# Performance work log

Measured on AMD Instinct MI355X. Metric: run time of the kernel, lower is better.

## Reference

```python
import jax, jax.numpy as jnp
import numpy as np

L, B, S, D, H = 4, 4, 2048, 512, 8
DH = D // H
FF = 4 * D
BN_EPS = 1e-3  # keras BatchNormalization default epsilon


def setup_inputs() -> dict:
    key = jax.random.key(0)
    ks = jax.random.split(key, 8)
    g = lambda k, shape: jax.random.normal(k, shape, dtype=jnp.float32) * 0.02
    return {
        "sequence": jax.random.normal(ks[0], (B, S, D), dtype=jnp.float32),
        "wq": g(ks[1], (L, D, D)), "bq": jnp.zeros((L, D), jnp.float32),
        "wk": g(ks[2], (L, D, D)), "bk": jnp.zeros((L, D), jnp.float32),
        "wv": g(ks[3], (L, D, D)), "bv": jnp.zeros((L, D), jnp.float32),
        "wo": g(ks[4], (L, D, D)), "bo": jnp.zeros((L, D), jnp.float32),
        "w1": g(ks[5], (L, D, FF)), "b1": jnp.zeros((L, FF), jnp.float32),
        "w2": g(ks[6], (L, FF, D)), "b2": jnp.zeros((L, D), jnp.float32),
        "g1": jnp.ones((L, D), jnp.float32), "be1": jnp.zeros((L, D), jnp.float32),
        "g2": jnp.ones((L, D), jnp.float32), "be2": jnp.zeros((L, D), jnp.float32),
    }


def reference(sequence, wq, bq, wk, bk, wv, bv, wo, bo, w1, b1, w2, b2, g1, be1, g2, be2):
    # Inference-mode BatchNorm with moving_mean=0, moving_var=1:
    # bn(x) = x / sqrt(1 + eps) * gamma + beta
    bn_inv = 1.0 / jnp.sqrt(jnp.float32(1.0 + BN_EPS))
    scale = 1.0 / jnp.sqrt(jnp.float32(DH))
    x = sequence  # [B, S, D]
    for i in range(L):
        # Batched multi-head self-attention (== the per-position loop concat)
        q = (x @ wq[i] + bq[i]).reshape(B, S, H, DH)
        k = (x @ wk[i] + bk[i]).reshape(B, S, H, DH)
        v = (x @ wv[i] + bv[i]).reshape(B, S, H, DH)
        att = jax.nn.softmax(jnp.einsum('bqhd,bkhd->bhqk', q, k) * scale, axis=-1)
        o = jnp.einsum('bhqk,bkhd->bqhd', att, v).reshape(B, S, D)
        o = o @ wo[i] + bo[i]
        x = (x + o) * bn_inv * g1[i] + be1[i]          # residual + BN
        f = jax.nn.relu(x @ w1[i] + b1[i]) @ w2[i] + b2[i]  # FFN
        x = (x + f) * bn_inv * g2[i] + be2[i]          # residual + BN
    return x
```

## Files before the change

kernel.cpp:

```cpp
#include <hip/hip_runtime.h>
#include <hip/hip_bf16.h>

#define BB   4
#define SS   2048
#define DDIM 512
#define HH   8
#define DHD  64
#define FFD  2048
#define LLN  4
#define NQKV 1536
#define BN_INV 0.9995003747f
#define QSCALE 0.18033688011112042f

typedef __bf16 bf16x8 __attribute__((ext_vector_type(8)));
typedef __bf16 bf16x4 __attribute__((ext_vector_type(4)));
typedef float  f32x4  __attribute__((ext_vector_type(4)));
typedef float  f32x16 __attribute__((ext_vector_type(16)));

__device__ __forceinline__ void gl2lds16(const void* g, void* l) {
  __builtin_amdgcn_global_load_lds((const __attribute__((address_space(1))) void*)g,
                                   (__attribute__((address_space(3))) void*)l, 16, 0, 0);
}

__device__ __forceinline__ unsigned pkbf16(float a, float b) {
  union { __bf16 h[2]; unsigned u; } x;
  x.h[0] = (__bf16)a; x.h[1] = (__bf16)b;
  return x.u;
}

__global__ __launch_bounds__(256) void k_transpose_w(const float* __restrict__ in,
                                                     __bf16* __restrict__ out,
                                                     int R, int C,
                                                     size_t in_zs, size_t out_zs) {
  __shared__ float tile[32][33];
  in += (size_t)blockIdx.z * in_zs;
  out += (size_t)blockIdx.z * out_zs;
  const int c0 = blockIdx.x * 32, r0 = blockIdx.y * 32;
  const int tx = threadIdx.x & 31, ty = threadIdx.x >> 5;
#pragma unroll
  for (int k = 0; k < 4; ++k) {
    int r = ty + k * 8;
    tile[r][tx] = in[(size_t)(r0 + r) * C + (c0 + tx)];
  }
  __syncthreads();
#pragma unroll
  for (int k = 0; k < 4; ++k) {
    int c = ty + k * 8;
    out[(size_t)(c0 + c) * R + (r0 + tx)] = (__bf16)tile[tx][c];
  }
}

__global__ __launch_bounds__(256) void k_bias_fuse(const float* __restrict__ bq,
                                                   const float* __restrict__ bk,
                                                   const float* __restrict__ bv,
                                                   float* __restrict__ out) {
  const int i = blockIdx.x * 256 + threadIdx.x;
  const int l = i / NQKV, j = i - l * NQKV;
  float v = (j < 512) ? bq[l * 512 + j]
          : (j < 1024) ? bk[l * 512 + j - 512]
                       : bv[l * 512 + j - 1024];
  out[i] = v;
}

__global__ __launch_bounds__(256) void k_transpose_v(const __bf16* __restrict__ qkv,
                                                     __bf16* __restrict__ vt) {
  __shared__ __bf16 tile[32][33];
  const int s0 = blockIdx.x * 32;
  const int d0 = blockIdx.y * 32;
  const int bh = blockIdx.z, b = bh >> 3, h = bh & 7;
  const int tx = threadIdx.x & 31, ty = threadIdx.x >> 5;
#pragma unroll
  for (int k = 0; k < 4; ++k) {
    int s = ty + k * 8;
    tile[s][tx] = qkv[(size_t)(b * SS + s0 + s) * NQKV + 2 * DDIM + h * DHD + d0 + tx];
  }
  __syncthreads();
#pragma unroll
  for (int k = 0; k < 4; ++k) {
    int d = ty + k * 8;
    vt[(size_t)(bh * DHD + d0 + d) * SS + (s0 + tx)] = tile[tx][d];
  }
}

__global__ __launch_bounds__(256) void k_cast(const float* __restrict__ in,
                                              float* __restrict__ xf,
                                              __bf16* __restrict__ xb) {
  const int i = (blockIdx.x * 256 + threadIdx.x) * 4;
  const float4 v = *(const float4*)(in + i);
  *(float4*)(xf + i) = v;
  bf16x4 o;
  o[0] = (__bf16)v.x; o[1] = (__bf16)v.y; o[2] = (__bf16)v.z; o[3] = (__bf16)v.w;
  *(bf16x4*)(xb + i) = o;
}

template <int EPI>
__global__ __launch_bounds__(256) void k_gemm_bt(const __bf16* __restrict__ A,
                                                 const __bf16* __restrict__ Bt,
                                                 const float* __restrict__ bias,
                                                 __bf16* __restrict__ Cb,
                                                 int M, int N, int K,
                                                 const float* __restrict__ xres,
                                                 float* __restrict__ xout,
                                                 const float* __restrict__ gvec,
                                                 const float* __restrict__ bvec) {
  __shared__ char As[2][16384];
  __shared__ char Bs[2][16384];
  const int tid = threadIdx.x;
  const int l = tid & 63, w = tid >> 6;
  const int wm = w >> 1, wn = w & 1;
  const int m0 = blockIdx.y * 128, n0 = blockIdx.x * 128;
  const int lr = l & 15, lg = l >> 4;
  f32x4 acc[4][4] = {};
  const int nk = K >> 6;
  const size_t ldab = (size_t)K * 2;

  auto stage = [&](int buf, int kt) {
    const int k0b = kt * 128;
#pragma unroll
    for (int i = 0; i < 4; ++i) {
      const int chunk = i * 256 + tid;
      const int row = chunk >> 3;
      const int scb = ((chunk & 7) * 16) ^ ((row & 7) << 4);
      gl2lds16((const char*)A + (size_t)(m0 + row) * ldab + k0b + scb,
               As[buf] + (i * 256 + w * 64) * 16);
      gl2lds16((const char*)Bt + (size_t)(n0 + row) * ldab + k0b + scb,
               Bs[buf] + (i * 256 + w * 64) * 16);
    }
  };

  stage(0, 0);
  __syncthreads();
  int cur = 0;
  for (int kt = 0; kt < nk; ++kt) {
    if (kt + 1 < nk) stage(cur ^ 1, kt + 1);
#pragma unroll
    for (int kk = 0; kk < 2; ++kk) {
      bf16x8 a[4], b[4];
#pragma unroll
      for (int m = 0; m < 4; ++m) {
        const int row = wm * 64 + m * 16 + lr;
        const int cb = kk * 64 + lg * 16;
        a[m] = *(const bf16x8*)(As[cur] + row * 128 + (cb ^ ((row & 7) << 4)));
      }
#pragma unroll
      for (int n = 0; n < 4; ++n) {
        const int row = wn * 64 + n * 16 + lr;
        const int cb = kk * 64 + lg * 16;
        b[n] = *(const bf16x8*)(Bs[cur] + row * 128 + (cb ^ ((row & 7) << 4)));
      }
#pragma unroll
      for (int m = 0; m < 4; ++m)
#pragma unroll
        for (int n = 0; n < 4; ++n)
          acc[m][n] = __builtin_amdgcn_mfma_f32_16x16x32_bf16(a[m], b[n], acc[m][n], 0, 0, 0);
    }
    asm volatile("s_waitcnt vmcnt(0)" ::: "memory");
    __syncthreads();
    cur ^= 1;
  }
#pragma unroll
  for (int m = 0; m < 4; ++m) {
    const int gm = m0 + wm * 64 + m * 16 + lg * 4;
#pragma unroll
    for (int n = 0; n < 4; ++n) {
      const int gn = n0 + wn * 64 + n * 16 + lr;
      const float bv_ = bias[gn];
#pragma unroll
      for (int j = 0; j < 4; ++j) {
        const size_t idx = (size_t)(gm + j) * N + gn;
        float v = acc[m][n][j] + bv_;
        if constexpr (EPI == 1) {
          Cb[idx] = (__bf16)fmaxf(v, 0.0f);
        } else if constexpr (EPI == 2) {
          float t = (xres[idx] + v) * BN_INV * gvec[gn] + bvec[gn];
          xout[idx] = t;
          Cb[idx] = (__bf16)t;
        } else {
          if (gn < DDIM) v *= QSCALE;
          Cb[idx] = (__bf16)v;
        }
      }
    }
  }
}

__global__ __launch_bounds__(256, 2) void k_attn(const __bf16* __restrict__ QKV,
                                                 const __bf16* __restrict__ Vt,
                                                 __bf16* __restrict__ O) {
  __shared__ char smem[65536];
  const int tid = threadIdx.x, l = tid & 63, w = tid >> 6;
  const int lq = l & 31, hi = l >> 5;
  const int f = blockIdx.y * 16 + blockIdx.x;
  const int L = (f & 7) * 64 + (f >> 3);
  const int qt = L & 15, bh = L >> 4;
  const int b = bh >> 3, h = bh & 7;
  const int myq = qt * 128 + w * 32 + lq;
  bf16x8 qf[4];
  {
    const __bf16* qp = QKV + (size_t)(b * SS + myq) * NQKV + h * DHD + hi * 8;
#pragma unroll
    for (int kc = 0; kc < 4; ++kc)
      qf[kc] = *(const bf16x8*)(qp + kc * 16);
  }
  f32x16 oaccT[2] = {};
  float rsum = 0.f;

  auto stage = [&](int buf, int t) {
    const int kv0 = t * 128;
    char* Kd = smem + buf * 16384;
    char* Vd = smem + 32768 + buf * 16384;
#pragma unroll
    for (int i = 0; i < 4; ++i) {
      const int chunk = i * 256 + tid;
      const int row = chunk >> 3;
      const int rs = row ^ ((((row >> 2) + 1) & 2) * 6);
      const int scb = ((chunk & 7) * 16) ^ ((row & 7) << 4);
      gl2lds16((const char*)QKV + ((size_t)(b * SS + kv0 + rs) * NQKV + DDIM + h * DHD) * 2 + scb,
               Kd + (i * 256 + w * 64) * 16);
    }
#pragma unroll
    for (int i = 0; i < 4; ++i) {
      const int chunk = i * 256 + tid;
      const int row = chunk >> 4;
      const int scb = ((chunk & 15) * 16) ^ ((row & 15) << 4);
      gl2lds16((const char*)Vt + ((size_t)(bh * DHD + row) * SS + kv0) * 2 + scb,
               Vd + (i * 256 + w * 64) * 16);
    }
  };

  stage(0, 0);
  __syncthreads();
  int cur = 0;
  for (int t = 0; t < SS / 128; ++t) {
    if (t < SS / 128 - 1) stage(cur ^ 1, t + 1);
    const char* Ks = smem + cur * 16384;
    const char* Vs = smem + 32768 + cur * 16384;
#pragma unroll
    for (int kt2 = 0; kt2 < 4; ++kt2) {
      const int krow = kt2 * 32 + lq;
      const int kswz = (krow & 7) << 4;
      f32x16 st = {};
      __builtin_amdgcn_s_setprio(1);
#pragma unroll
      for (int kc = 0; kc < 4; ++kc) {
        bf16x8 kf = *(const bf16x8*)(Ks + krow * 128 + ((kc * 32 + hi * 16) ^ kswz));
        st = __builtin_amdgcn_mfma_f32_32x32x16_bf16(kf, qf[kc], st, 0, 0, 0);
      }
      __builtin_amdgcn_s_setprio(0);
      unsigned pk8[8];
#pragma unroll
      for (int i = 0; i < 8; ++i) {
        const float e0 = __builtin_amdgcn_exp2f(st[2 * i]);
        const float e1 = __builtin_amdgcn_exp2f(st[2 * i + 1]);
        rsum += e0 + e1;
        pk8[i] = pkbf16(e0, e1);
      }
      union { unsigned u[4]; bf16x8 v; } pf0, pf1;
#pragma unroll
      for (int i = 0; i < 4; ++i) { pf0.u[i] = pk8[i]; pf1.u[i] = pk8[4 + i]; }
      __builtin_amdgcn_s_setprio(1);
#pragma unroll
      for (int dt = 0; dt < 2; ++dt) {
        const int vrow = dt * 32 + lq;
        const int vswz = (vrow & 15) << 4;
        bf16x8 vf0 = *(const bf16x8*)(Vs + vrow * 256 + ((kt2 * 64 + hi * 16) ^ vswz));
        bf16x8 vf1 = *(const bf16x8*)(Vs + vrow * 256 + ((kt2 * 64 + 32 + hi * 16) ^ vswz));
        oaccT[dt] = __builtin_amdgcn_mfma_f32_32x32x16_bf16(vf0, pf0.v, oaccT[dt], 0, 0, 0);
        oaccT[dt] = __builtin_amdgcn_mfma_f32_32x32x16_bf16(vf1, pf1.v, oaccT[dt], 0, 0, 0);
      }
      __builtin_amdgcn_s_setprio(0);
    }
    asm volatile("s_waitcnt vmcnt(0)" ::: "memory");
    __syncthreads();
    cur ^= 1;
  }
  rsum += __shfl_xor(rsum, 32);
  const float inv = 1.0f / rsum;
  __bf16* op = O + (size_t)(b * SS + myq) * DDIM + h * DHD;
#pragma unroll
  for (int dt = 0; dt < 2; ++dt)
#pragma unroll
    for (int g = 0; g < 4; ++g) {
      const int d0 = dt * 32 + g * 8 + hi * 4;
      unsigned u0 = pkbf16(oaccT[dt][4 * g + 0] * inv, oaccT[dt][4 * g + 1] * inv);
      unsigned u1 = pkbf16(oaccT[dt][4 * g + 2] * inv, oaccT[dt][4 * g + 3] * inv);
      uint2 uu; uu.x = u0; uu.y = u1;
      *(uint2*)(op + d0) = uu;
    }
}

static constexpr size_t SZ_WQKVT = (size_t)LLN * NQKV * DDIM * 2;
static constexpr size_t SZ_WOT   = (size_t)LLN * DDIM * DDIM * 2;
static constexpr size_t SZ_WT_DF = (size_t)LLN * DDIM * FFD * 2;
static constexpr size_t SZ_BQKV  = (size_t)LLN * NQKV * 4;
static constexpr size_t SZ_X     = (size_t)BB * SS * DDIM * 4;
static constexpr size_t SZ_ABF   = (size_t)BB * SS * DDIM * 2;
static constexpr size_t SZ_QKV   = (size_t)BB * SS * NQKV * 2;
static constexpr size_t OFF_WQKVT = 0;
static constexpr size_t OFF_WOT  = OFF_WQKVT + SZ_WQKVT;
static constexpr size_t OFF_W1T  = OFF_WOT + SZ_WOT;
static constexpr size_t OFF_W2T  = OFF_W1T + SZ_WT_DF;
static constexpr size_t OFF_BQKV = OFF_W2T + SZ_WT_DF;
static constexpr size_t OFF_X    = OFF_BQKV + SZ_BQKV;
static constexpr size_t OFF_XB   = OFF_X + SZ_X;
static constexpr size_t OFF_QKV  = OFF_XB + SZ_ABF;
static constexpr size_t OFF_VT   = OFF_QKV + SZ_QKV;
static constexpr size_t OFF_OB   = OFF_VT + SZ_ABF;
static constexpr size_t OFF_H1   = OFF_QKV;

extern "C" void kernel_launch(void* const* d_in, const int* in_sizes, int n_in,
                              void* d_out, int out_size, void* d_ws, size_t ws_size,
                              hipStream_t stream) {
  const float* seq = (const float*)d_in[0];
  const float* wq = (const float*)d_in[1];  const float* bq = (const float*)d_in[2];
  const float* wk = (const float*)d_in[3];  const float* bk = (const float*)d_in[4];
  const float* wv = (const float*)d_in[5];  const float* bv = (const float*)d_in[6];
  const float* wo = (const float*)d_in[7];  const float* bo = (const float*)d_in[8];
  const float* w1 = (const float*)d_in[9];  const float* b1 = (const float*)d_in[10];
  const float* w2 = (const float*)d_in[11]; const float* b2 = (const float*)d_in[12];
  const float* g1 = (const float*)d_in[13]; const float* be1 = (const float*)d_in[14];
  const float* g2 = (const float*)d_in[15]; const float* be2 = (const float*)d_in[16];

  char* ws = (char*)d_ws;
  __bf16* wqkvt = (__bf16*)(ws + OFF_WQKVT);
  __bf16* wot = (__bf16*)(ws + OFF_WOT);
  __bf16* w1t = (__bf16*)(ws + OFF_W1T);
  __bf16* w2t = (__bf16*)(ws + OFF_W2T);
  float*  bqkv = (float*)(ws + OFF_BQKV);
  float*  xf  = (float*)(ws + OFF_X);
  __bf16* xb  = (__bf16*)(ws + OFF_XB);
  __bf16* qkvb = (__bf16*)(ws + OFF_QKV);
  __bf16* vtb = (__bf16*)(ws + OFF_VT);
  __bf16* ob  = (__bf16*)(ws + OFF_OB);
  __bf16* h1  = (__bf16*)(ws + OFF_H1);

  const size_t zDD = (size_t)DDIM * DDIM;
  const size_t zQKV = (size_t)NQKV * DDIM;
  const size_t zDF = (size_t)DDIM * FFD;
  k_transpose_w<<<dim3(16, 16, LLN), 256, 0, stream>>>(wq, wqkvt, DDIM, DDIM, zDD, zQKV);
  k_transpose_w<<<dim3(16, 16, LLN), 256, 0, stream>>>(wk, wqkvt + (size_t)DDIM * DDIM, DDIM, DDIM, zDD, zQKV);
  k_transpose_w<<<dim3(16, 16, LLN), 256, 0, stream>>>(wv, wqkvt + (size_t)2 * DDIM * DDIM, DDIM, DDIM, zDD, zQKV);
  k_transpose_w<<<dim3(16, 16, LLN), 256, 0, stream>>>(wo, wot, DDIM, DDIM, zDD, zDD);
  k_transpose_w<<<dim3(64, 16, LLN), 256, 0, stream>>>(w1, w1t, DDIM, FFD, zDF, zDF);
  k_transpose_w<<<dim3(16, 64, LLN), 256, 0, stream>>>(w2, w2t, FFD, DDIM, zDF, zDF);
  k_bias_fuse<<<LLN * NQKV / 256, 256, 0, stream>>>(bq, bk, bv, bqkv);
  k_cast<<<4096, 256, 0, stream>>>(seq, xf, xb);

  const int M = BB * SS;
  for (int i = 0; i < LLN; ++i) {
    k_gemm_bt<3><<<dim3(NQKV / 128, M / 128), 256, 0, stream>>>(
        xb, wqkvt + (size_t)i * NQKV * DDIM, bqkv + i * NQKV, qkvb, M, NQKV, DDIM,
        nullptr, nullptr, nullptr, nullptr);
    k_transpose_v<<<dim3(SS / 32, DHD / 32, BB * HH), 256, 0, stream>>>(qkvb, vtb);
    k_attn<<<dim3(SS / 128, BB * HH), 256, 0, stream>>>(qkvb, vtb, ob);
    k_gemm_bt<2><<<dim3(DDIM / 128, M / 128), 256, 0, stream>>>(
        ob, wot + (size_t)i * DDIM * DDIM, bo + i * DDIM, xb, M, DDIM, DDIM,
        xf, xf, g1 + i * DDIM, be1 + i * DDIM);
    k_gemm_bt<1><<<dim3(FFD / 128, M / 128), 256, 0, stream>>>(
        xb, w1t + (size_t)i * DDIM * FFD, b1 + i * FFD, h1, M, FFD, DDIM,
        nullptr, nullptr, nullptr, nullptr);
    k_gemm_bt<2><<<dim3(DDIM / 128, M / 128), 256, 0, stream>>>(
        h1, w2t + (size_t)i * DDIM * FFD, b2 + i * DDIM, xb, M, DDIM, FFD,
        xf, (i == LLN - 1) ? (float*)d_out : xf, g2 + i * DDIM, be2 + i * DDIM);
  }
  (void)in_sizes; (void)n_in; (void)out_size; (void)ws_size;
}
```

Before: 642.5 us.

## Shrink GEMM N-tile to 64, add XCD block swizzle, rework K LDS swizzle, fuse transposes

Result: faster. 594.8 us (-7.4%).

```diff
diff --git a/kernel.cpp b/kernel.cpp
--- a/kernel.cpp
+++ b/kernel.cpp
@@ -28,6 +28,42 @@
   return x.u;
 }
 
+__device__ __forceinline__ int2 xcd_swz(void) {
+  const int f = blockIdx.y * gridDim.x + blockIdx.x;
+  const int q = (gridDim.x * gridDim.y) >> 3;
+  const int L = (f & 7) * q + (f >> 3);
+  int2 r; r.x = L % gridDim.x; r.y = L / gridDim.x;
+  return r;
+}
+
+__global__ __launch_bounds__(256) void k_transpose_w4(const float* __restrict__ wq,
+                                                      const float* __restrict__ wk,
+                                                      const float* __restrict__ wv,
+                                                      const float* __restrict__ wo,
+                                                      __bf16* __restrict__ wqkvt,
+                                                      __bf16* __restrict__ wot) {
+  __shared__ float tile[32][33];
+  const int z = blockIdx.z, widx = z >> 2, layer = z & 3;
+  const float* in = (widx == 0) ? wq : (widx == 1) ? wk : (widx == 2) ? wv : wo;
+  in += (size_t)layer * DDIM * DDIM;
+  __bf16* out = (widx < 3)
+      ? wqkvt + (size_t)layer * NQKV * DDIM + (size_t)widx * DDIM * DDIM
+      : wot + (size_t)layer * DDIM * DDIM;
+  const int c0 = blockIdx.x * 32, r0 = blockIdx.y * 32;
+  const int tx = threadIdx.x & 31, ty = threadIdx.x >> 5;
+#pragma unroll
+  for (int k = 0; k < 4; ++k) {
+    int r = ty + k * 8;
+    tile[r][tx] = in[(size_t)(r0 + r) * DDIM + (c0 + tx)];
+  }
+  __syncthreads();
+#pragma unroll
+  for (int k = 0; k < 4; ++k) {
+    int c = ty + k * 8;
+    out[(size_t)(c0 + c) * DDIM + (r0 + tx)] = (__bf16)tile[tx][c];
+  }
+}
+
 __global__ __launch_bounds__(256) void k_transpose_w(const float* __restrict__ in,
                                                      __bf16* __restrict__ out,
                                                      int R, int C,
@@ -94,23 +130,24 @@
 }
 
 template <int EPI>
-__global__ __launch_bounds__(256) void k_gemm_bt(const __bf16* __restrict__ A,
-                                                 const __bf16* __restrict__ Bt,
-                                                 const float* __restrict__ bias,
-                                                 __bf16* __restrict__ Cb,
-                                                 int M, int N, int K,
-                                                 const float* __restrict__ xres,
-                                                 float* __restrict__ xout,
-                                                 const float* __restrict__ gvec,
-                                                 const float* __restrict__ bvec) {
-  __shared__ char As[2][16384];
-  __shared__ char Bs[2][16384];
+__global__ __launch_bounds__(256, 3) void k_gemm_bt(const __bf16* __restrict__ A,
+                                                    const __bf16* __restrict__ Bt,
+                                                    const float* __restrict__ bias,
+                                                    __bf16* __restrict__ Cb,
+                                                    int M, int N, int K,
+                                                    const float* __restrict__ xres,
+                                                    float* __restrict__ xout,
+                                                    const float* __restrict__ gvec,
+                                                    const float* __restrict__ bvec) {
+  __shared__ __align__(16) char As[2][16384];
+  __shared__ __align__(16) char Bs[2][8192];
   const int tid = threadIdx.x;
   const int l = tid & 63, w = tid >> 6;
   const int wm = w >> 1, wn = w & 1;
-  const int m0 = blockIdx.y * 128, n0 = blockIdx.x * 128;
+  const int2 bxy = xcd_swz();
+  const int m0 = bxy.y * 128, n0 = bxy.x * 64;
   const int lr = l & 15, lg = l >> 4;
-  f32x4 acc[4][4] = {};
+  f32x4 acc[4][2] = {};
   const int nk = K >> 6;
   const size_t ldab = (size_t)K * 2;
 
@@ -123,6 +160,12 @@
       const int scb = ((chunk & 7) * 16) ^ ((row & 7) << 4);
       gl2lds16((const char*)A + (size_t)(m0 + row) * ldab + k0b + scb,
                As[buf] + (i * 256 + w * 64) * 16);
+    }
+#pragma unroll
+    for (int i = 0; i < 2; ++i) {
+      const int chunk = i * 256 + tid;
+      const int row = chunk >> 3;
+      const int scb = ((chunk & 7) * 16) ^ ((row & 7) << 4);
       gl2lds16((const char*)Bt + (size_t)(n0 + row) * ldab + k0b + scb,
                Bs[buf] + (i * 256 + w * 64) * 16);
     }
@@ -135,7 +178,7 @@
     if (kt + 1 < nk) stage(cur ^ 1, kt + 1);
 #pragma unroll
     for (int kk = 0; kk < 2; ++kk) {
-      bf16x8 a[4], b[4];
+      bf16x8 a[4], b[2];
 #pragma unroll
       for (int m = 0; m < 4; ++m) {
         const int row = wm * 64 + m * 16 + lr;
@@ -143,15 +186,15 @@
         a[m] = *(const bf16x8*)(As[cur] + row * 128 + (cb ^ ((row & 7) << 4)));
       }
 #pragma unroll
-      for (int n = 0; n < 4; ++n) {
-        const int row = wn * 64 + n * 16 + lr;
+      for (int n = 0; n < 2; ++n) {
+        const int row = wn * 32 + n * 16 + lr;
         const int cb = kk * 64 + lg * 16;
         b[n] = *(const bf16x8*)(Bs[cur] + row * 128 + (cb ^ ((row & 7) << 4)));
       }
 #pragma unroll
       for (int m = 0; m < 4; ++m)
 #pragma unroll
-        for (int n = 0; n < 4; ++n)
+        for (int n = 0; n < 2; ++n)
           acc[m][n] = __builtin_amdgcn_mfma_f32_16x16x32_bf16(a[m], b[n], acc[m][n], 0, 0, 0);
     }
     asm volatile("s_waitcnt vmcnt(0)" ::: "memory");
@@ -162,8 +205,8 @@
   for (int m = 0; m < 4; ++m) {
     const int gm = m0 + wm * 64 + m * 16 + lg * 4;
 #pragma unroll
-    for (int n = 0; n < 4; ++n) {
-      const int gn = n0 + wn * 64 + n * 16 + lr;
+    for (int n = 0; n < 2; ++n) {
+      const int gn = n0 + wn * 32 + n * 16 + lr;
       const float bv_ = bias[gn];
 #pragma unroll
       for (int j = 0; j < 4; ++j) {
@@ -212,10 +255,14 @@
 #pragma unroll
     for (int i = 0; i < 4; ++i) {
       const int chunk = i * 256 + tid;
-      const int row = chunk >> 3;
-      const int rs = row ^ ((((row >> 2) + 1) & 2) * 6);
-      const int scb = ((chunk & 7) * 16) ^ ((row & 7) << 4);
-      gl2lds16((const char*)QKV + ((size_t)(b * SS + kv0 + rs) * NQKV + DDIM + h * DHD) * 2 + scb,
+      const int p = chunk >> 4, s = chunk & 15;
+      const int r2 = p << 1;
+      const int x = s ^ (r2 & 15);
+      const int hb = x >> 3;
+      const int r = r2 + hb;
+      const int c16 = (x ^ hb) & 7;
+      const int rs = r ^ ((((r >> 2) + 1) & 2) * 6);
+      gl2lds16((const char*)QKV + ((size_t)(b * SS + kv0 + rs) * NQKV + DDIM + h * DHD) * 2 + c16 * 16,
                Kd + (i * 256 + w * 64) * 16);
     }
 #pragma unroll
@@ -238,12 +285,15 @@
 #pragma unroll
     for (int kt2 = 0; kt2 < 4; ++kt2) {
       const int krow = kt2 * 32 + lq;
-      const int kswz = (krow & 7) << 4;
+      const int kline = krow >> 1;
+      const int kbase = (krow & 1) << 3;
+      const int kmask = krow & 15;
       f32x16 st = {};
       __builtin_amdgcn_s_setprio(1);
 #pragma unroll
       for (int kc = 0; kc < 4; ++kc) {
-        bf16x8 kf = *(const bf16x8*)(Ks + krow * 128 + ((kc * 32 + hi * 16) ^ kswz));
+        const int sl = (kbase + kc * 2 + hi) ^ kmask;
+        bf16x8 kf = *(const bf16x8*)(Ks + kline * 256 + (sl << 4));
         st = __builtin_amdgcn_mfma_f32_32x32x16_bf16(kf, qf[kc], st, 0, 0, 0);
       }
       __builtin_amdgcn_s_setprio(0);
@@ -334,13 +384,8 @@
   __bf16* ob  = (__bf16*)(ws + OFF_OB);
   __bf16* h1  = (__bf16*)(ws + OFF_H1);
 
-  const size_t zDD = (size_t)DDIM * DDIM;
-  const size_t zQKV = (size_t)NQKV * DDIM;
   const size_t zDF = (size_t)DDIM * FFD;
-  k_transpose_w<<<dim3(16, 16, LLN), 256, 0, stream>>>(wq, wqkvt, DDIM, DDIM, zDD, zQKV);
-  k_transpose_w<<<dim3(16, 16, LLN), 256, 0, stream>>>(wk, wqkvt + (size_t)DDIM * DDIM, DDIM, DDIM, zDD, zQKV);
-  k_transpose_w<<<dim3(16, 16, LLN), 256, 0, stream>>>(wv, wqkvt + (size_t)2 * DDIM * DDIM, DDIM, DDIM, zDD, zQKV);
-  k_transpose_w<<<dim3(16, 16, LLN), 256, 0, stream>>>(wo, wot, DDIM, DDIM, zDD, zDD);
+  k_transpose_w4<<<dim3(16, 16, 16), 256, 0, stream>>>(wq, wk, wv, wo, wqkvt, wot);
   k_transpose_w<<<dim3(64, 16, LLN), 256, 0, stream>>>(w1, w1t, DDIM, FFD, zDF, zDF);
   k_transpose_w<<<dim3(16, 64, LLN), 256, 0, stream>>>(w2, w2t, FFD, DDIM, zDF, zDF);
   k_bias_fuse<<<LLN * NQKV / 256, 256, 0, stream>>>(bq, bk, bv, bqkv);
@@ -348,18 +393,18 @@
 
   const int M = BB * SS;
   for (int i = 0; i < LLN; ++i) {
-    k_gemm_bt<3><<<dim3(NQKV / 128, M / 128), 256, 0, stream>>>(
+    k_gemm_bt<3><<<dim3(NQKV / 64, M / 128), 256, 0, stream>>>(
         xb, wqkvt + (size_t)i * NQKV * DDIM, bqkv + i * NQKV, qkvb, M, NQKV, DDIM,
         nullptr, nullptr, nullptr, nullptr);
     k_transpose_v<<<dim3(SS / 32, DHD / 32, BB * HH), 256, 0, stream>>>(qkvb, vtb);
     k_attn<<<dim3(SS / 128, BB * HH), 256, 0, stream>>>(qkvb, vtb, ob);
-    k_gemm_bt<2><<<dim3(DDIM / 128, M / 128), 256, 0, stream>>>(
+    k_gemm_bt<2><<<dim3(DDIM / 64, M / 128), 256, 0, stream>>>(
         ob, wot + (size_t)i * DDIM * DDIM, bo + i * DDIM, xb, M, DDIM, DDIM,
         xf, xf, g1 + i * DDIM, be1 + i * DDIM);
-    k_gemm_bt<1><<<dim3(FFD / 128, M / 128), 256, 0, stream>>>(
+    k_gemm_bt<1><<<dim3(FFD / 64, M / 128), 256, 0, stream>>>(
         xb, w1t + (size_t)i * DDIM * FFD, b1 + i * FFD, h1, M, FFD, DDIM,
         nullptr, nullptr, nullptr, nullptr);
-    k_gemm_bt<2><<<dim3(DDIM / 128, M / 128), 256, 0, stream>>>(
+    k_gemm_bt<2><<<dim3(DDIM / 64, M / 128), 256, 0, stream>>>(
         h1, w2t + (size_t)i * DDIM * FFD, b2 + i * DDIM, xb, M, DDIM, FFD,
         xf, (i == LLN - 1) ? (float*)d_out : xf, g2 + i * DDIM, be2 + i * DDIM);
   }
```
